# Performance work log

Hardware: AMD Instinct MI355X
Metric: run time of the kernel (lower is better)

## Reference

```python
import jax, jax.numpy as jnp
import numpy as np


def setup_inputs() -> dict:
    key = jax.random.key(0)
    kq, kk, kv = jax.random.split(key, 3)
    shape = (2, 16, 2048, 64)  # [B, H, S, D]
    return {
        "q": jax.random.normal(kq, shape, dtype=jnp.float32),
        "k": jax.random.normal(kk, shape, dtype=jnp.float32),
        "v": jax.random.normal(kv, shape, dtype=jnp.float32),
    }


def reference(q, k, v):
    # scores = q @ k^T / sqrt(d_k)  -> [B, H, S, S]
    d_k = k.shape[-1]
    scale = 1.0 / jnp.sqrt(jnp.asarray(d_k, dtype=q.dtype))
    scores = jnp.einsum("bhqd,bhkd->bhqk", q, k) * scale
    seq_len = q.shape[-2]
    # causal mask: position q attends to k <= q
    causal = jnp.tril(jnp.ones((seq_len, seq_len), dtype=bool))
    scores = jnp.where(causal, scores, jnp.asarray(-jnp.inf, dtype=scores.dtype))
    probs = jax.nn.softmax(scores, axis=-1)
    return jnp.einsum("bhqk,bhkd->bhqd", probs, v)
```

## Files before the change

### kernel.cpp

```cpp
#include <hip/hip_runtime.h>
#include <hip/hip_bf16.h>

typedef short bf16x8 __attribute__((ext_vector_type(8)));
typedef short bf16x4 __attribute__((ext_vector_type(4)));
typedef float f32x4  __attribute__((ext_vector_type(4)));
typedef float f32x16 __attribute__((ext_vector_type(16)));

#define D_DIM 64
#define SEQ 2048
#define BHD (SEQ * D_DIM)
#define SCALE_L2E 0.1803368801111204f

__device__ __forceinline__ unsigned short f2bf(float f) {
    unsigned u = __builtin_bit_cast(unsigned, f);
    u += 0x7fffu + ((u >> 16) & 1u);
    return (unsigned short)(u >> 16);
}

__device__ __forceinline__ unsigned swz(unsigned row, unsigned colByte) {
    return (row * 128u + colByte) ^ ((row & 7u) << 4);
}

__device__ __forceinline__ void gl_lds(const unsigned short* g, unsigned char* lds_generic,
                                       unsigned lds_off) {
    __builtin_amdgcn_global_load_lds(
        (const __attribute__((address_space(1))) void*)g,
        (__attribute__((address_space(3))) void*)(lds_generic + lds_off), 16, 0, 0);
}

__device__ __forceinline__ float fexp2(float x) {
    float r; asm("v_exp_f32 %0, %1" : "=v"(r) : "v"(x)); return r;
}
__device__ __forceinline__ unsigned cvtpk(float lo, float hi) {
    unsigned r; asm("v_cvt_pk_bf16_f32 %0, %1, %2" : "=v"(r) : "v"(lo), "v"(hi)); return r;
}

__global__ __launch_bounds__(256) void prep_kernel(const float* __restrict__ K,
                                                   const float* __restrict__ V,
                                                   unsigned short* __restrict__ Kb,
                                                   unsigned short* __restrict__ Vt) {
    __shared__ unsigned short t[64][66];
    const int st = blockIdx.x;
    const int bh = blockIdx.y;
    const int tid = threadIdx.x;
    const size_t base = (size_t)bh * BHD;

    const float* ksrc = K + base + st * 4096;
    unsigned short* kdst = Kb + base + st * 4096;
    #pragma unroll
    for (int j = 0; j < 2; ++j) {
        int e = (j * 256 + tid) * 8;
        float4 a = *(const float4*)(ksrc + e);
        float4 b = *(const float4*)(ksrc + e + 4);
        bf16x8 o;
        o[0] = (short)f2bf(a.x); o[1] = (short)f2bf(a.y);
        o[2] = (short)f2bf(a.z); o[3] = (short)f2bf(a.w);
        o[4] = (short)f2bf(b.x); o[5] = (short)f2bf(b.y);
        o[6] = (short)f2bf(b.z); o[7] = (short)f2bf(b.w);
        *(bf16x8*)(kdst + e) = o;
    }

    const float* vb = V + base + st * 64 * D_DIM;
    #pragma unroll
    for (int j = 0; j < 4; ++j) {
        int n = tid + 256 * j;
        int r = n >> 4;
        int c = (n & 15) << 2;
        float4 v = *(const float4*)(vb + r * D_DIM + c);
        t[r][c + 0] = f2bf(v.x); t[r][c + 1] = f2bf(v.y);
        t[r][c + 2] = f2bf(v.z); t[r][c + 3] = f2bf(v.w);
    }
    __syncthreads();
    #pragma unroll
    for (int j = 0; j < 2; ++j) {
        int m = tid + 256 * j;
        int d = m >> 3;
        int s8 = (m & 7) << 3;
        bf16x8 o;
        #pragma unroll
        for (int e = 0; e < 8; ++e) o[e] = (short)t[s8 + e][d];
        *(bf16x8*)(Vt + base + (size_t)d * SEQ + st * 64 + s8) = o;
    }
}

__global__ __launch_bounds__(512, 2) void attn_fwd(const float* __restrict__ Qp,
                                                   const unsigned short* __restrict__ Kb,
                                                   const unsigned short* __restrict__ Vtb,
                                                   float* __restrict__ Op) {
    __shared__ __align__(16) unsigned char lds[65536];

    int id = blockIdx.y * gridDim.x + blockIdx.x;
    int wid = (id & 7) * 32 + (id >> 3);
    const int i  = wid & 7;
    const int bh = wid >> 3;

    const int tid  = threadIdx.x;
    const int w    = tid >> 6;
    const int lane = tid & 63;
    const int l31  = lane & 31;
    const int hi2  = lane >> 5;
    const int wsub = w & 3;
    const int qt   = (w >> 2) ? (15 - i) : i;
    const int qlo  = qt * 128 + wsub * 32;
    const int t_w  = qlo >> 6;
    const int TB   = 32 - 2 * i;

    const size_t base = (size_t)bh * BHD;
    const float* qp = Qp + base;
    const unsigned short* kb = Kb + base;
    const unsigned short* vt = Vtb + base;
    float* op = Op + base;

    const int srow = tid >> 3;
    const int scb  = ((tid & 7) << 4) ^ ((srow & 7) << 4);
    const int kOff = srow * D_DIM + (scb >> 1);
    const int vOff = srow * SEQ + (scb >> 1);
    const unsigned sdst = (unsigned)w * 1024u;

    auto STAGE = [&](int buf, int t) {
        unsigned bb = (unsigned)buf * 16384u;
        gl_lds(kb + (size_t)t * 4096 + kOff, lds, bb + sdst);
        gl_lds(vt + (size_t)t * 64 + vOff, lds, bb + 8192u + sdst);
    };

    const float* qsrc = qp + (size_t)(qlo + l31) * D_DIM + hi2 * 8;
    float4 qraw[8];
    #pragma unroll
    for (int dk = 0; dk < 4; ++dk) {
        qraw[2 * dk]     = *(const float4*)(qsrc + dk * 16);
        qraw[2 * dk + 1] = *(const float4*)(qsrc + dk * 16 + 4);
    }
    STAGE(0, 0);
    STAGE(1, 1);

    bf16x8 qB[4];
    #pragma unroll
    for (int dk = 0; dk < 4; ++dk) {
        float4 a = qraw[2 * dk], b = qraw[2 * dk + 1];
        bf16x8 v;
        v[0] = (short)f2bf(a.x * SCALE_L2E); v[1] = (short)f2bf(a.y * SCALE_L2E);
        v[2] = (short)f2bf(a.z * SCALE_L2E); v[3] = (short)f2bf(a.w * SCALE_L2E);
        v[4] = (short)f2bf(b.x * SCALE_L2E); v[5] = (short)f2bf(b.y * SCALE_L2E);
        v[6] = (short)f2bf(b.z * SCALE_L2E); v[7] = (short)f2bf(b.w * SCALE_L2E);
        qB[dk] = v;
    }

    f32x16 acc0 = {}, acc1 = {};
    float m_r = -3.0e38f, l_r = 0.f;
    bf16x8 pf[4];
    const int qg = qlo + l31;

    #pragma unroll 1
    for (int t = 0; t < TB; ++t) {
        if (t < TB - 1) asm volatile("s_waitcnt vmcnt(2)" ::: "memory");
        else            asm volatile("s_waitcnt vmcnt(0)" ::: "memory");
        __builtin_amdgcn_s_barrier();
        __builtin_amdgcn_sched_barrier(0);
        if (t + 2 < TB) STAGE((t + 2) & 3, t + 2);

        const bool act = (t <= t_w);
        const bool pvp = (t >= 1) && (t - 1 <= t_w);

        f32x16 st0 = {}, st1 = {};
        if (act) {
            const unsigned kbuf = (unsigned)(t & 3) * 16384u;
            __builtin_amdgcn_s_setprio(1);
            #pragma unroll
            for (int dk = 0; dk < 4; ++dk) {
                bf16x8 k0 = *(const bf16x8*)&lds[kbuf +
                    swz((unsigned)l31, (unsigned)(dk * 32 + hi2 * 16))];
                bf16x8 k1 = *(const bf16x8*)&lds[kbuf +
                    swz((unsigned)(32 + l31), (unsigned)(dk * 32 + hi2 * 16))];
                st0 = __builtin_amdgcn_mfma_f32_32x32x16_bf16(k0, qB[dk], st0, 0, 0, 0);
                st1 = __builtin_amdgcn_mfma_f32_32x32x16_bf16(k1, qB[dk], st1, 0, 0, 0);
            }
            __builtin_amdgcn_s_setprio(0);
        }

        if (pvp) {
            const unsigned vbuf = (unsigned)((t - 1) & 3) * 16384u + 8192u;
            __builtin_amdgcn_s_setprio(1);
            #pragma unroll
            for (int mm = 0; mm < 4; ++mm) {
                bf16x8 va0 = *(const bf16x8*)&lds[vbuf +
                    swz((unsigned)l31, (unsigned)(mm * 32 + hi2 * 16))];
                bf16x8 va1 = *(const bf16x8*)&lds[vbuf +
                    swz((unsigned)(32 + l31), (unsigned)(mm * 32 + hi2 * 16))];
                acc0 = __builtin_amdgcn_mfma_f32_32x32x16_bf16(va0, pf[mm], acc0, 0, 0, 0);
                acc1 = __builtin_amdgcn_mfma_f32_32x32x16_bf16(va1, pf[mm], acc1, 0, 0, 0);
            }
            __builtin_amdgcn_s_setprio(0);
        }

        if (act) {
            if (t == t_w) {
                #pragma unroll
                for (int r = 0; r < 16; ++r) {
                    int kvb = t * 64 + (r & 3) + 8 * (r >> 2) + 4 * hi2;
                    if (kvb > qg)      st0[r] = -3.0e38f;
                    if (kvb + 32 > qg) st1[r] = -3.0e38f;
                }
            }

            float m8[8];
            #pragma unroll
            for (int r = 0; r < 8; ++r)
                m8[r] = fmaxf(fmaxf(st0[r], st0[r + 8]), fmaxf(st1[r], st1[r + 8]));
            #pragma unroll
            for (int r = 0; r < 4; ++r) m8[r] = fmaxf(m8[r], m8[r + 4]);
            float mx = fmaxf(fmaxf(m8[0], m8[1]), fmaxf(m8[2], m8[3]));
            mx = fmaxf(mx, __shfl_xor(mx, 32));

            float mn;
            if (__all(mx <= m_r + 8.0f)) {
                mn = m_r;
            } else {
                mn = fmaxf(m_r, mx);
                float sc = fexp2(m_r - mn);
                m_r = mn;
                l_r *= sc;
                #pragma unroll
                for (int r = 0; r < 16; ++r) { acc0[r] *= sc; acc1[r] *= sc; }
            }

            float p[32];
            #pragma unroll
            for (int r = 0; r < 16; ++r) p[r] = fexp2(st0[r] - mn);
            #pragma unroll
            for (int r = 0; r < 16; ++r) p[16 + r] = fexp2(st1[r] - mn);
            float s16[16];
            #pragma unroll
            for (int r = 0; r < 16; ++r) s16[r] = p[r] + p[16 + r];
            #pragma unroll
            for (int r = 0; r < 8; ++r) s16[r] += s16[r + 8];
            #pragma unroll
            for (int r = 0; r < 4; ++r) s16[r] += s16[r + 4];
            float rs = (s16[0] + s16[1]) + (s16[2] + s16[3]);
            rs += __shfl_xor(rs, 32);
            l_r += rs;

            #pragma unroll
            for (int b2 = 0; b2 < 2; ++b2) {
                unsigned W[4][2];
                #pragma unroll
                for (int c = 0; c < 4; ++c) {
                    W[c][0] = cvtpk(p[b2 * 16 + 4 * c + 0], p[b2 * 16 + 4 * c + 1]);
                    W[c][1] = cvtpk(p[b2 * 16 + 4 * c + 2], p[b2 * 16 + 4 * c + 3]);
                }
                #pragma unroll
                for (int m = 0; m < 2; ++m) {
                    unsigned s0 = hi2 ? W[2 * m][0] : W[2 * m + 1][0];
                    unsigned s1 = hi2 ? W[2 * m][1] : W[2 * m + 1][1];
                    unsigned r0 = (unsigned)__shfl_xor((int)s0, 32);
                    unsigned r1 = (unsigned)__shfl_xor((int)s1, 32);
                    int4 fw;
                    fw.x = (int)(hi2 ? r0 : W[2 * m][0]);
                    fw.y = (int)(hi2 ? r1 : W[2 * m][1]);
                    fw.z = (int)(hi2 ? W[2 * m + 1][0] : r0);
                    fw.w = (int)(hi2 ? W[2 * m + 1][1] : r1);
                    pf[b2 * 2 + m] = __builtin_bit_cast(bf16x8, fw);
                }
            }
        }
    }

    if (t_w == TB - 1) {
        const unsigned vbuf = (unsigned)((TB - 1) & 3) * 16384u + 8192u;
        #pragma unroll
        for (int mm = 0; mm < 4; ++mm) {
            bf16x8 va0 = *(const bf16x8*)&lds[vbuf +
                swz((unsigned)l31, (unsigned)(mm * 32 + hi2 * 16))];
            bf16x8 va1 = *(const bf16x8*)&lds[vbuf +
                swz((unsigned)(32 + l31), (unsigned)(mm * 32 + hi2 * 16))];
            acc0 = __builtin_amdgcn_mfma_f32_32x32x16_bf16(va0, pf[mm], acc0, 0, 0, 0);
            acc1 = __builtin_amdgcn_mfma_f32_32x32x16_bf16(va1, pf[mm], acc1, 0, 0, 0);
        }
    }

    float inv = 1.f / l_r;
    #pragma unroll
    for (int c = 0; c < 4; ++c) {
        float4 o;
        o.x = acc0[4 * c + 0] * inv; o.y = acc0[4 * c + 1] * inv;
        o.z = acc0[4 * c + 2] * inv; o.w = acc0[4 * c + 3] * inv;
        *(float4*)(op + (size_t)qg * D_DIM + 8 * c + 4 * hi2) = o;
    }
    #pragma unroll
    for (int c = 0; c < 4; ++c) {
        float4 o;
        o.x = acc1[4 * c + 0] * inv; o.y = acc1[4 * c + 1] * inv;
        o.z = acc1[4 * c + 2] * inv; o.w = acc1[4 * c + 3] * inv;
        *(float4*)(op + (size_t)qg * D_DIM + 32 + 8 * c + 4 * hi2) = o;
    }
}

__global__ __launch_bounds__(256) void attn_fwd_fb(
    const float* __restrict__ Qp, const float* __restrict__ Kp,
    const float* __restrict__ Vp, float* __restrict__ Op, int S)
{
    __shared__ __align__(16) unsigned char lds_k[64 * 128];
    __shared__ __align__(16) unsigned char lds_vt[64 * 128];
    __shared__ __align__(16) unsigned char lds_p[4 * 16 * 128];

    const int qt = blockIdx.x, bh = blockIdx.y, tid = threadIdx.x;
    const int w = tid >> 6, lane = tid & 63, lo = lane & 15, hi = lane >> 4;
    const size_t base = (size_t)bh * S * D_DIM;
    const float* qp = Qp + base; const float* kp = Kp + base;
    const float* vp = Vp + base; float* op = Op + base;
    const int qw = qt * 64 + w * 16;

    auto swzl = [](unsigned row, unsigned colByte) {
        return (row * 128u + colByte) ^ ((row & 7u) << 4);
    };

    bf16x8 qf[2];
    {
        const float* src = qp + (size_t)(qw + lo) * D_DIM + hi * 8;
        #pragma unroll
        for (int f = 0; f < 2; ++f) {
            float4 a = *(const float4*)(src + f * 32);
            float4 b = *(const float4*)(src + f * 32 + 4);
            bf16x8 v;
            v[0] = (short)f2bf(a.x * 0.125f); v[1] = (short)f2bf(a.y * 0.125f);
            v[2] = (short)f2bf(a.z * 0.125f); v[3] = (short)f2bf(a.w * 0.125f);
            v[4] = (short)f2bf(b.x * 0.125f); v[5] = (short)f2bf(b.y * 0.125f);
            v[6] = (short)f2bf(b.z * 0.125f); v[7] = (short)f2bf(b.w * 0.125f);
            qf[f] = v;
        }
    }
    f32x4 o_acc[4]; float m_r[4], l_r[4];
    #pragma unroll
    for (int r = 0; r < 4; ++r) { m_r[r] = -__builtin_inff(); l_r[r] = 0.f; }
    #pragma unroll
    for (int dt = 0; dt < 4; ++dt) o_acc[dt] = (f32x4){0.f, 0.f, 0.f, 0.f};
    const unsigned pbase = (unsigned)w * 2048u;

    for (int t = 0; t <= qt; ++t) {
        const size_t kv0 = (size_t)t * 64;
        __syncthreads();
        #pragma unroll
        for (int jj = 0; jj < 4; ++jj) {
            int n = tid + 256 * jj;
            int r = n >> 4, c = (n & 15) << 2;
            float4 kk = *(const float4*)(kp + (kv0 + r) * D_DIM + c);
            bf16x4 kbv;
            kbv[0] = (short)f2bf(kk.x); kbv[1] = (short)f2bf(kk.y);
            kbv[2] = (short)f2bf(kk.z); kbv[3] = (short)f2bf(kk.w);
            *(bf16x4*)&lds_k[swzl((unsigned)r, (unsigned)c * 2)] = kbv;
            float4 vv = *(const float4*)(vp + (kv0 + r) * D_DIM + c);
            *(unsigned short*)&lds_vt[swzl((unsigned)(c + 0), (unsigned)r * 2)] = f2bf(vv.x);
            *(unsigned short*)&lds_vt[swzl((unsigned)(c + 1), (unsigned)r * 2)] = f2bf(vv.y);
            *(unsigned short*)&lds_vt[swzl((unsigned)(c + 2), (unsigned)r * 2)] = f2bf(vv.z);
            *(unsigned short*)&lds_vt[swzl((unsigned)(c + 3), (unsigned)r * 2)] = f2bf(vv.w);
        }
        __syncthreads();

        float sc[4][4];
        #pragma unroll
        for (int kc = 0; kc < 4; ++kc) {
            f32x4 s = (f32x4){0.f, 0.f, 0.f, 0.f};
            #pragma unroll
            for (int f = 0; f < 2; ++f) {
                bf16x8 kfv = *(const bf16x8*)&lds_k[swzl((unsigned)(kc * 16 + lo),
                                                         (unsigned)(hi * 16 + f * 64))];
                s = __builtin_amdgcn_mfma_f32_16x16x32_bf16(qf[f], kfv, s, 0, 0, 0);
            }
            #pragma unroll
            for (int r = 0; r < 4; ++r) sc[kc][r] = s[r];
        }
        if (t == qt) {
            #pragma unroll
            for (int kc = 0; kc < 4; ++kc)
                #pragma unroll
                for (int r = 0; r < 4; ++r) {
                    int qg2 = w * 16 + hi * 4 + r, kg = kc * 16 + lo;
                    if (kg > qg2) sc[kc][r] = -__builtin_inff();
                }
        }
        float scale[4];
        #pragma unroll
        for (int r = 0; r < 4; ++r) {
            float mx = fmaxf(fmaxf(sc[0][r], sc[1][r]), fmaxf(sc[2][r], sc[3][r]));
            mx = fmaxf(mx, __shfl_xor(mx, 1)); mx = fmaxf(mx, __shfl_xor(mx, 2));
            mx = fmaxf(mx, __shfl_xor(mx, 4)); mx = fmaxf(mx, __shfl_xor(mx, 8));
            float mn = fmaxf(m_r[r], mx);
            scale[r] = __expf(m_r[r] - mn); m_r[r] = mn;
            float s0 = 0.f;
            #pragma unroll
            for (int kc = 0; kc < 4; ++kc) {
                float pv = __expf(sc[kc][r] - mn); sc[kc][r] = pv; s0 += pv;
            }
            s0 += __shfl_xor(s0, 1); s0 += __shfl_xor(s0, 2);
            s0 += __shfl_xor(s0, 4); s0 += __shfl_xor(s0, 8);
            l_r[r] = l_r[r] * scale[r] + s0;
        }
        #pragma unroll
        for (int r = 0; r < 4; ++r) {
            unsigned qr = (unsigned)(hi * 4 + r);
            #pragma unroll
            for (int kc = 0; kc < 4; ++kc)
                *(unsigned short*)&lds_p[pbase + swzl(qr, (unsigned)((kc * 16 + lo) * 2))] =
                    f2bf(sc[kc][r]);
            #pragma unroll
            for (int dt = 0; dt < 4; ++dt) o_acc[dt][r] *= scale[r];
        }
        bf16x8 pa0 = *(const bf16x8*)&lds_p[pbase + swzl((unsigned)lo, (unsigned)(hi * 16))];
        bf16x8 pa1 = *(const bf16x8*)&lds_p[pbase + swzl((unsigned)lo, (unsigned)(hi * 16 + 64))];
        #pragma unroll
        for (int dt = 0; dt < 4; ++dt) {
            bf16x8 vb0 = *(const bf16x8*)&lds_vt[swzl((unsigned)(dt * 16 + lo), (unsigned)(hi * 16))];
            bf16x8 vb1 = *(const bf16x8*)&lds_vt[swzl((unsigned)(dt * 16 + lo), (unsigned)(hi * 16 + 64))];
            o_acc[dt] = __builtin_amdgcn_mfma_f32_16x16x32_bf16(pa0, vb0, o_acc[dt], 0, 0, 0);
            o_acc[dt] = __builtin_amdgcn_mfma_f32_16x16x32_bf16(pa1, vb1, o_acc[dt], 0, 0, 0);
        }
    }
    const int qrow = qw + hi * 4;
    #pragma unroll
    for (int r = 0; r < 4; ++r) {
        float inv = 1.f / l_r[r];
        #pragma unroll
        for (int dt = 0; dt < 4; ++dt)
            op[(size_t)(qrow + r) * D_DIM + dt * 16 + lo] = o_acc[dt][r] * inv;
    }
}

extern "C" void kernel_launch(void* const* d_in, const int* in_sizes, int n_in,
                              void* d_out, int out_size, void* d_ws, size_t ws_size,
                              hipStream_t stream) {
    const float* q = (const float*)d_in[0];
    const float* k = (const float*)d_in[1];
    const float* v = (const float*)d_in[2];
    float* o = (float*)d_out;

    const size_t nelem = (size_t)32 * BHD;
    const size_t need = 2 * nelem * sizeof(unsigned short);

    if (ws_size >= need) {
        unsigned short* kbf = (unsigned short*)d_ws;
        unsigned short* vtb = kbf + nelem;
        prep_kernel<<<dim3(32, 32), 256, 0, stream>>>(k, v, kbf, vtb);
        attn_fwd<<<dim3(8, 32), 512, 0, stream>>>(q, kbf, vtb, o);
    } else {
        attn_fwd_fb<<<dim3(32, 32), 256, 0, stream>>>(q, k, v, o, SEQ);
    }
}
```

Measured before the change: 59.74 us.

## Split KV range across wave halves and merge partial softmax via LDS

Each block now handles one 128-row query tile instead of a balanced pair, doubling the grid. The two wave groups process alternating KV tiles (even and odd), and their partial accumulators, maxima and sums are merged through LDS at the end. The separate QK/PV software pipeline is replaced by an in-iteration QK→softmax→PV sequence with a two-buffer stage that loads two KV tiles per step, and the occupancy hint is raised. This trades the previous pairing-based load balancing and cross-iteration overlap for more blocks and split-KV parallelism, at the cost of an extra LDS reduction and a full vmcnt(0) wait every iteration.

```diff
diff --git a/kernel.cpp b/kernel.cpp
--- a/kernel.cpp
+++ b/kernel.cpp
@@ -83,16 +83,17 @@
     }
 }
 
-__global__ __launch_bounds__(512, 2) void attn_fwd(const float* __restrict__ Qp,
+__global__ __launch_bounds__(512, 4) void attn_fwd(const float* __restrict__ Qp,
                                                    const unsigned short* __restrict__ Kb,
                                                    const unsigned short* __restrict__ Vtb,
                                                    float* __restrict__ Op) {
     __shared__ __align__(16) unsigned char lds[65536];
 
     int id = blockIdx.y * gridDim.x + blockIdx.x;
-    int wid = (id & 7) * 32 + (id >> 3);
-    const int i  = wid & 7;
-    const int bh = wid >> 3;
+    int j  = id >> 3;
+    const int bh = (id & 7) * 4 + (j >> 4);
+    const int jq = j & 15;
+    const int qtile = (j < 32) ? (15 - jq) : jq;
 
     const int tid  = threadIdx.x;
     const int w    = tid >> 6;
@@ -100,10 +101,12 @@
     const int l31  = lane & 31;
     const int hi2  = lane >> 5;
     const int wsub = w & 3;
-    const int qt   = (w >> 2) ? (15 - i) : i;
-    const int qlo  = qt * 128 + wsub * 32;
-    const int t_w  = qlo >> 6;
-    const int TB   = 32 - 2 * i;
+    const int par  = w >> 2;
+
+    const int qlo = qtile * 128 + wsub * 32;
+    const int t_w = qlo >> 6;
+    const int qg  = qlo + l31;
+    const int nt  = qtile + 1;
 
     const size_t base = (size_t)bh * BHD;
     const float* qp = Qp + base;
@@ -115,23 +118,26 @@
     const int scb  = ((tid & 7) << 4) ^ ((srow & 7) << 4);
     const int kOff = srow * D_DIM + (scb >> 1);
     const int vOff = srow * SEQ + (scb >> 1);
-    const unsigned sdst = (unsigned)w * 1024u;
-
-    auto STAGE = [&](int buf, int t) {
-        unsigned bb = (unsigned)buf * 16384u;
-        gl_lds(kb + (size_t)t * 4096 + kOff, lds, bb + sdst);
-        gl_lds(vt + (size_t)t * 64 + vOff, lds, bb + 8192u + sdst);
+    const unsigned sdst = (unsigned)tid * 16u;
+
+    auto STAGE = [&](int it) {
+        unsigned bb = (unsigned)(it & 1) * 32768u;
+        const unsigned short* kg = kb + (size_t)(2 * it) * 4096 + kOff;
+        const unsigned short* vg = vt + (size_t)(2 * it) * 64 + vOff;
+        gl_lds(kg, lds, bb + sdst);
+        gl_lds(vg, lds, bb + 8192u + sdst);
+        gl_lds(kg + 4096, lds, bb + 16384u + sdst);
+        gl_lds(vg + 64, lds, bb + 24576u + sdst);
     };
 
-    const float* qsrc = qp + (size_t)(qlo + l31) * D_DIM + hi2 * 8;
+    const float* qsrc = qp + (size_t)qg * D_DIM + hi2 * 8;
     float4 qraw[8];
     #pragma unroll
     for (int dk = 0; dk < 4; ++dk) {
         qraw[2 * dk]     = *(const float4*)(qsrc + dk * 16);
         qraw[2 * dk + 1] = *(const float4*)(qsrc + dk * 16 + 4);
     }
-    STAGE(0, 0);
-    STAGE(1, 1);
+    STAGE(0);
 
     bf16x8 qB[4];
     #pragma unroll
@@ -147,23 +153,20 @@
 
     f32x16 acc0 = {}, acc1 = {};
     float m_r = -3.0e38f, l_r = 0.f;
-    bf16x8 pf[4];
-    const int qg = qlo + l31;
 
     #pragma unroll 1
-    for (int t = 0; t < TB; ++t) {
-        if (t < TB - 1) asm volatile("s_waitcnt vmcnt(2)" ::: "memory");
-        else            asm volatile("s_waitcnt vmcnt(0)" ::: "memory");
+    for (int it = 0; it < nt; ++it) {
+        asm volatile("s_waitcnt vmcnt(0)" ::: "memory");
         __builtin_amdgcn_s_barrier();
         __builtin_amdgcn_sched_barrier(0);
-        if (t + 2 < TB) STAGE((t + 2) & 3, t + 2);
-
-        const bool act = (t <= t_w);
-        const bool pvp = (t >= 1) && (t - 1 <= t_w);
-
-        f32x16 st0 = {}, st1 = {};
-        if (act) {
-            const unsigned kbuf = (unsigned)(t & 3) * 16384u;
+        if (it + 1 < nt) STAGE(it + 1);
+
+        const int tile = 2 * it + par;
+        if (tile <= t_w) {
+            const unsigned kbuf = (unsigned)(it & 1) * 32768u + (unsigned)par * 16384u;
+            const unsigned vbuf = kbuf + 8192u;
+
+            f32x16 st0 = {}, st1 = {};
             __builtin_amdgcn_s_setprio(1);
             #pragma unroll
             for (int dk = 0; dk < 4; ++dk) {
@@ -175,28 +178,11 @@
                 st1 = __builtin_amdgcn_mfma_f32_32x32x16_bf16(k1, qB[dk], st1, 0, 0, 0);
             }
             __builtin_amdgcn_s_setprio(0);
-        }
-
-        if (pvp) {
-            const unsigned vbuf = (unsigned)((t - 1) & 3) * 16384u + 8192u;
-            __builtin_amdgcn_s_setprio(1);
-            #pragma unroll
-            for (int mm = 0; mm < 4; ++mm) {
-                bf16x8 va0 = *(const bf16x8*)&lds[vbuf +
-                    swz((unsigned)l31, (unsigned)(mm * 32 + hi2 * 16))];
-                bf16x8 va1 = *(const bf16x8*)&lds[vbuf +
-                    swz((unsigned)(32 + l31), (unsigned)(mm * 32 + hi2 * 16))];
-                acc0 = __builtin_amdgcn_mfma_f32_32x32x16_bf16(va0, pf[mm], acc0, 0, 0, 0);
-                acc1 = __builtin_amdgcn_mfma_f32_32x32x16_bf16(va1, pf[mm], acc1, 0, 0, 0);
-            }
-            __builtin_amdgcn_s_setprio(0);
-        }
-
-        if (act) {
-            if (t == t_w) {
+
+            if (tile == t_w) {
                 #pragma unroll
                 for (int r = 0; r < 16; ++r) {
-                    int kvb = t * 64 + (r & 3) + 8 * (r >> 2) + 4 * hi2;
+                    int kvb = tile * 64 + (r & 3) + 8 * (r >> 2) + 4 * hi2;
                     if (kvb > qg)      st0[r] = -3.0e38f;
                     if (kvb + 32 > qg) st1[r] = -3.0e38f;
                 }
@@ -223,14 +209,13 @@
                 for (int r = 0; r < 16; ++r) { acc0[r] *= sc; acc1[r] *= sc; }
             }
 
-            float p[32];
-            #pragma unroll
-            for (int r = 0; r < 16; ++r) p[r] = fexp2(st0[r] - mn);
-            #pragma unroll
-            for (int r = 0; r < 16; ++r) p[16 + r] = fexp2(st1[r] - mn);
+            #pragma unroll
+            for (int r = 0; r < 16; ++r) st0[r] = fexp2(st0[r] - mn);
+            #pragma unroll
+            for (int r = 0; r < 16; ++r) st1[r] = fexp2(st1[r] - mn);
             float s16[16];
             #pragma unroll
-            for (int r = 0; r < 16; ++r) s16[r] = p[r] + p[16 + r];
+            for (int r = 0; r < 16; ++r) s16[r] = st0[r] + st1[r];
             #pragma unroll
             for (int r = 0; r < 8; ++r) s16[r] += s16[r + 8];
             #pragma unroll
@@ -239,13 +224,18 @@
             rs += __shfl_xor(rs, 32);
             l_r += rs;
 
+            bf16x8 pf[4];
             #pragma unroll
             for (int b2 = 0; b2 < 2; ++b2) {
                 unsigned W[4][2];
                 #pragma unroll
                 for (int c = 0; c < 4; ++c) {
-                    W[c][0] = cvtpk(p[b2 * 16 + 4 * c + 0], p[b2 * 16 + 4 * c + 1]);
-                    W[c][1] = cvtpk(p[b2 * 16 + 4 * c + 2], p[b2 * 16 + 4 * c + 3]);
+                    float v0 = b2 ? st1[4 * c + 0] : st0[4 * c + 0];
+                    float v1 = b2 ? st1[4 * c + 1] : st0[4 * c + 1];
+                    float v2 = b2 ? st1[4 * c + 2] : st0[4 * c + 2];
+                    float v3 = b2 ? st1[4 * c + 3] : st0[4 * c + 3];
+                    W[c][0] = cvtpk(v0, v1);
+                    W[c][1] = cvtpk(v2, v3);
                 }
                 #pragma unroll
                 for (int m = 0; m < 2; ++m) {
@@ -261,36 +251,59 @@
                     pf[b2 * 2 + m] = __builtin_bit_cast(bf16x8, fw);
                 }
             }
-        }
-    }
-
-    if (t_w == TB - 1) {
-        const unsigned vbuf = (unsigned)((TB - 1) & 3) * 16384u + 8192u;
-        #pragma unroll
-        for (int mm = 0; mm < 4; ++mm) {
-            bf16x8 va0 = *(const bf16x8*)&lds[vbuf +
-                swz((unsigned)l31, (unsigned)(mm * 32 + hi2 * 16))];
-            bf16x8 va1 = *(const bf16x8*)&lds[vbuf +
-                swz((unsigned)(32 + l31), (unsigned)(mm * 32 + hi2 * 16))];
-            acc0 = __builtin_amdgcn_mfma_f32_32x32x16_bf16(va0, pf[mm], acc0, 0, 0, 0);
-            acc1 = __builtin_amdgcn_mfma_f32_32x32x16_bf16(va1, pf[mm], acc1, 0, 0, 0);
-        }
-    }
-
-    float inv = 1.f / l_r;
-    #pragma unroll
-    for (int c = 0; c < 4; ++c) {
-        float4 o;
-        o.x = acc0[4 * c + 0] * inv; o.y = acc0[4 * c + 1] * inv;
-        o.z = acc0[4 * c + 2] * inv; o.w = acc0[4 * c + 3] * inv;
-        *(float4*)(op + (size_t)qg * D_DIM + 8 * c + 4 * hi2) = o;
-    }
-    #pragma unroll
-    for (int c = 0; c < 4; ++c) {
-        float4 o;
-        o.x = acc1[4 * c + 0] * inv; o.y = acc1[4 * c + 1] * inv;
-        o.z = acc1[4 * c + 2] * inv; o.w = acc1[4 * c + 3] * inv;
-        *(float4*)(op + (size_t)qg * D_DIM + 32 + 8 * c + 4 * hi2) = o;
+
+            __builtin_amdgcn_s_setprio(1);
+            #pragma unroll
+            for (int mm = 0; mm < 4; ++mm) {
+                bf16x8 va0 = *(const bf16x8*)&lds[vbuf +
+                    swz((unsigned)l31, (unsigned)(mm * 32 + hi2 * 16))];
+                bf16x8 va1 = *(const bf16x8*)&lds[vbuf +
+                    swz((unsigned)(32 + l31), (unsigned)(mm * 32 + hi2 * 16))];
+                acc0 = __builtin_amdgcn_mfma_f32_32x32x16_bf16(va0, pf[mm], acc0, 0, 0, 0);
+                acc1 = __builtin_amdgcn_mfma_f32_32x32x16_bf16(va1, pf[mm], acc1, 0, 0, 0);
+            }
+            __builtin_amdgcn_s_setprio(0);
+        }
+    }
+
+    __builtin_amdgcn_s_barrier();
+    const unsigned mbase = (unsigned)wsub * (64u * 144u) + (unsigned)lane * 144u;
+    if (w >= 4) {
+        #pragma unroll
+        for (int c = 0; c < 4; ++c) {
+            f32x4 q0 = {acc0[4 * c], acc0[4 * c + 1], acc0[4 * c + 2], acc0[4 * c + 3]};
+            *(f32x4*)&lds[mbase + c * 16] = q0;
+            f32x4 q1 = {acc1[4 * c], acc1[4 * c + 1], acc1[4 * c + 2], acc1[4 * c + 3]};
+            *(f32x4*)&lds[mbase + 64 + c * 16] = q1;
+        }
+        *(float*)&lds[mbase + 128] = m_r;
+        *(float*)&lds[mbase + 132] = l_r;
+    }
+    __builtin_amdgcn_s_barrier();
+    if (w < 4) {
+        float m2 = *(const float*)&lds[mbase + 128];
+        float l2 = *(const float*)&lds[mbase + 132];
+        float m  = fmaxf(m_r, m2);
+        float a1 = fexp2(m_r - m);
+        float a2 = fexp2(m2 - m);
+        float l  = a1 * l_r + a2 * l2;
+        float inv = 1.f / l;
+        #pragma unroll
+        for (int c = 0; c < 4; ++c) {
+            f32x4 p0 = *(const f32x4*)&lds[mbase + c * 16];
+            f32x4 p1 = *(const f32x4*)&lds[mbase + 64 + c * 16];
+            float4 o0, o1;
+            o0.x = (a1 * acc0[4 * c + 0] + a2 * p0[0]) * inv;
+            o0.y = (a1 * acc0[4 * c + 1] + a2 * p0[1]) * inv;
+            o0.z = (a1 * acc0[4 * c + 2] + a2 * p0[2]) * inv;
+            o0.w = (a1 * acc0[4 * c + 3] + a2 * p0[3]) * inv;
+            o1.x = (a1 * acc1[4 * c + 0] + a2 * p1[0]) * inv;
+            o1.y = (a1 * acc1[4 * c + 1] + a2 * p1[1]) * inv;
+            o1.z = (a1 * acc1[4 * c + 2] + a2 * p1[2]) * inv;
+            o1.w = (a1 * acc1[4 * c + 3] + a2 * p1[3]) * inv;
+            *(float4*)(op + (size_t)qg * D_DIM + 8 * c + 4 * hi2) = o0;
+            *(float4*)(op + (size_t)qg * D_DIM + 32 + 8 * c + 4 * hi2) = o1;
+        }
     }
 }
 
@@ -439,7 +452,7 @@
         unsigned short* kbf = (unsigned short*)d_ws;
         unsigned short* vtb = kbf + nelem;
         prep_kernel<<<dim3(32, 32), 256, 0, stream>>>(k, v, kbf, vtb);
-        attn_fwd<<<dim3(8, 32), 512, 0, stream>>>(q, kbf, vtb, o);
+        attn_fwd<<<dim3(16, 32), 512, 0, stream>>>(q, kbf, vtb, o);
     } else {
         attn_fwd_fb<<<dim3(32, 32), 256, 0, stream>>>(q, k, v, o, SEQ);
     }
```

New measurement: 49.74 us. -16.7%, faster.
